# Kernel tuning notes

Hardware: AMD Instinct MI355X
Metric: run time of the kernel (lower is better)

The kernel has to match this reference:

```python
import jax, jax.numpy as jnp
import numpy as np

DIM = 768        # channel dim C
HEADS = 12       # num_heads
MAXLEN = 128     # max_seq_len == window length N
NW = 64          # num_windows
B = 4            # batch


def setup_inputs() -> dict:
    key = jax.random.key(0)
    k0, k1, k2, k3 = jax.random.split(key, 4)
    B_ = NW * B
    x = jax.random.normal(k0, (B_, MAXLEN, DIM), jnp.float32)
    mask = jnp.zeros((NW, MAXLEN, MAXLEN), jnp.float32)  # 0/-inf additive window mask
    qkv_w = jax.random.normal(k1, (3 * DIM, DIM), jnp.float32) * 0.02
    bias_table = jax.random.normal(k2, (2 * MAXLEN - 1, HEADS), jnp.float32) * 0.02
    proj_w = jax.random.normal(k3, (DIM, DIM), jnp.float32) * 0.02
    proj_b = jnp.zeros((DIM,), jnp.float32)
    return {"x": x, "mask": mask, "qkv_w": qkv_w, "bias_table": bias_table,
            "proj_w": proj_w, "proj_b": proj_b}


def reference(x, mask, qkv_w, bias_table, proj_w, proj_b):
    B_, N, C = x.shape
    H = HEADS
    hd = C // H
    scale = hd ** -0.5
    # qkv projection (no bias): (B_, N, 3, H, hd)
    qkv = (x @ qkv_w.T).reshape(B_, N, 3, H, hd)
    q = qkv[:, :, 0].transpose(0, 2, 1, 3) * scale  # (B_, H, N, hd)
    k = qkv[:, :, 1].transpose(0, 2, 1, 3)
    v = qkv[:, :, 2].transpose(0, 2, 1, 3)
    attn = jnp.einsum('bhnd,bhmd->bhnm', q, k)       # (B_, H, N, N)
    # relative position bias gather
    coords = jnp.arange(N)
    rel_idx = coords[:, None] - coords[None, :] + (MAXLEN - 1)  # (N, N)
    bias = bias_table[rel_idx]                        # (N, N, H)
    attn = attn + bias.transpose(2, 0, 1)[None]       # (B_, H, N, N)
    # window mask add (mask ndim == 3 branch)
    nW = mask.shape[0]
    attn = attn.reshape(B_ // nW, nW, H, N, N) + mask[None, :, None]
    attn = jax.nn.softmax(attn.reshape(B_, H, N, N), axis=-1)
    out = jnp.einsum('bhnm,bhmd->bhnd', attn, v)      # (B_, H, N, hd)
    out = out.transpose(0, 2, 1, 3).reshape(B_, N, C)
    return out @ proj_w.T + proj_b
```

## Files before the change

kernel.cpp:

```cpp
#include <hip/hip_runtime.h>
#include <hip/hip_bf16.h>
#include <stdint.h>

typedef unsigned short u16;
typedef __bf16 bf16x8 __attribute__((ext_vector_type(8)));
typedef float f32x4 __attribute__((ext_vector_type(4)));

__device__ __forceinline__ u16 f2bf(float f) {
  union { float f; uint32_t u; } v; v.f = f;
  uint32_t u = v.u;
  return (u16)((u + 0x7FFFu + ((u >> 16) & 1u)) >> 16);
}

__device__ __forceinline__ f32x4 mfma16(bf16x8 a, bf16x8 b, f32x4 c) {
  return __builtin_amdgcn_mfma_f32_16x16x32_bf16(a, b, c, 0, 0, 0);
}

#define GLOBAL_TO_LDS16(g, l)                                                  \
  __builtin_amdgcn_global_load_lds(                                            \
      (const __attribute__((address_space(1))) void*)(g),                      \
      (__attribute__((address_space(3))) void*)(l), 16, 0, 0)

__device__ __forceinline__ int xcd_swz(int lin, int nwg) {
  return (lin & 7) * (nwg >> 3) + (lin >> 3);
}

__global__ void cvt_bf16_all(const float* __restrict__ x, u16* __restrict__ xb,
                             const float* __restrict__ qw, u16* __restrict__ qwb,
                             const float* __restrict__ pw, u16* __restrict__ pwb) {
  int blk = blockIdx.x;
  const float* src; u16* dst; int i;
  if (blk < 24576)        { src = x;  dst = xb;  i = blk * 256 + threadIdx.x; }
  else if (blk < 26304)   { src = qw; dst = qwb; i = (blk - 24576) * 256 + threadIdx.x; }
  else                    { src = pw; dst = pwb; i = (blk - 26304) * 256 + threadIdx.x; }
  float4 f = ((const float4*)src)[i];
  ushort4 o;
  o.x = f2bf(f.x); o.y = f2bf(f.y); o.z = f2bf(f.z); o.w = f2bf(f.w);
  ((ushort4*)dst)[i] = o;
}

template <bool SWAP>
__global__ __launch_bounds__(256) void qkv_gemm(
    const u16* __restrict__ A, const u16* __restrict__ Bt, int nbase,
    u16* __restrict__ q, u16* __restrict__ k, u16* __restrict__ vT) {
  const int K = 768;
  __shared__ u16 As[128 * 64];
  __shared__ u16 Bs[128 * 64];
  int tid = threadIdx.x;
  int wave = tid >> 6, lane = tid & 63;
  int quad = lane >> 4, lrow = lane & 15;
  int lin = blockIdx.x + gridDim.x * blockIdx.y;
  int swz = xcd_swz(lin, gridDim.x * gridDim.y);
  int bx = swz % gridDim.x, by = swz / gridDim.x;
  int m0 = by * 128, n0 = nbase + bx * 128;
  int wr = (wave >> 1) * 64, wc = (wave & 1) * 64;

  const u16* asrc[4]; const u16* bsrc[4]; int ldst[4];
#pragma unroll
  for (int s = 0; s < 4; s++) {
    int p = (wave * 4 + s) * 64 + lane;
    int row = p >> 3, cp = p & 7;
    int c = cp ^ (row & 7);
    asrc[s] = A + (size_t)(m0 + row) * K + c * 8;
    bsrc[s] = Bt + (size_t)(n0 + row) * K + c * 8;
    ldst[s] = p * 8;
  }
  f32x4 acc[4][4] = {};
  for (int k0 = 0; k0 < K; k0 += 64) {
#pragma unroll
    for (int s = 0; s < 4; s++) {
      GLOBAL_TO_LDS16(asrc[s] + k0, As + ldst[s]);
      GLOBAL_TO_LDS16(bsrc[s] + k0, Bs + ldst[s]);
    }
    __syncthreads();
#pragma unroll
    for (int kk = 0; kk < 2; kk++) {
      bf16x8 am[4], bn[4];
#pragma unroll
      for (int i = 0; i < 4; i++) {
        int r = wr + i * 16 + lrow;
        am[i] = *(const bf16x8*)(As + r * 64 + ((((kk << 2) | quad) ^ (r & 7)) << 3));
      }
#pragma unroll
      for (int j = 0; j < 4; j++) {
        int r = wc + j * 16 + lrow;
        bn[j] = *(const bf16x8*)(Bs + r * 64 + ((((kk << 2) | quad) ^ (r & 7)) << 3));
      }
#pragma unroll
      for (int i = 0; i < 4; i++)
#pragma unroll
        for (int j = 0; j < 4; j++)
          acc[i][j] = SWAP ? mfma16(bn[i], am[j], acc[i][j])
                           : mfma16(am[i], bn[j], acc[i][j]);
    }
    __syncthreads();
  }
  int b = m0 >> 7;
  if (SWAP) {
    int t = n0 / 768;
    float s = (t == 0) ? 0.125f : 1.0f;
    u16* dst = (t == 0) ? q : k;
#pragma unroll
    for (int i = 0; i < 4; i++) {
      int nb = (n0 - t * 768) + wc + i * 16 + quad * 4;
      int h = nb >> 6, d0 = nb & 63;
#pragma unroll
      for (int j = 0; j < 4; j++) {
        int seq = wr + j * 16 + lrow;
        ushort4 o;
        o.x = f2bf(acc[i][j][0] * s); o.y = f2bf(acc[i][j][1] * s);
        o.z = f2bf(acc[i][j][2] * s); o.w = f2bf(acc[i][j][3] * s);
        *(ushort4*)(dst + ((size_t)(b * 12 + h)) * 8192 + seq * 64 + d0) = o;
      }
    }
  } else {
#pragma unroll
    for (int j = 0; j < 4; j++) {
      int nb = (n0 - 1536) + wc + j * 16 + lrow;
      int h = nb >> 6, d = nb & 63;
#pragma unroll
      for (int i = 0; i < 4; i++) {
        int seq0 = wr + i * 16 + quad * 4;
        ushort4 o;
        o.x = f2bf(acc[i][j][0]); o.y = f2bf(acc[i][j][1]);
        o.z = f2bf(acc[i][j][2]); o.w = f2bf(acc[i][j][3]);
        *(ushort4*)(vT + ((size_t)(b * 12 + h)) * 8192 + d * 128 + seq0) = o;
      }
    }
  }
}

__global__ __launch_bounds__(512) void attn_kernel(
    const u16* __restrict__ q, const u16* __restrict__ k, const u16* __restrict__ vT,
    const float* __restrict__ mask, const float* __restrict__ bias_table,
    u16* __restrict__ attn_out) {
  __shared__ u16 smem[2 * 128 * 64];
  __shared__ u16 vTs[64 * 128];
  __shared__ float bias_s[255];
  u16* qs = smem;
  u16* ks = smem + 128 * 64;
  u16* ps = smem;
  int tid = threadIdx.x;
  int wave = tid >> 6, lane = tid & 63;
  int quad = lane >> 4, lrow = lane & 15;
  int bh = xcd_swz(blockIdx.x, gridDim.x);
  int b = bh / 12, h = bh - b * 12;
  int w = b & 63;
  if (tid < 255) bias_s[tid] = bias_table[tid * 12 + h];
  const u16* qg = q + (size_t)bh * 8192;
  const u16* kg = k + (size_t)bh * 8192;
  const u16* vg = vT + (size_t)bh * 8192;
#pragma unroll
  for (int s = 0; s < 2; s++) {
    int p = s * 512 + tid;
    int row = p >> 3, c = (p & 7) ^ (row & 7);
    GLOBAL_TO_LDS16(qg + row * 64 + c * 8, qs + p * 8);
    GLOBAL_TO_LDS16(kg + row * 64 + c * 8, ks + p * 8);
    int dd = p >> 4, cv = (p & 15) ^ (dd & 7);
    GLOBAL_TO_LDS16(vg + dd * 128 + cv * 8, vTs + p * 8);
  }
  __syncthreads();

  int row = wave * 16 + lrow;
  f32x4 sacc[8] = {};
#pragma unroll
  for (int kk = 0; kk < 2; kk++) {
    bf16x8 qf = *(const bf16x8*)(qs + row * 64 + ((((kk << 2) | quad) ^ (row & 7)) << 3));
#pragma unroll
    for (int i = 0; i < 8; i++) {
      int rk = i * 16 + lrow;
      bf16x8 kf = *(const bf16x8*)(ks + rk * 64 + ((((kk << 2) | quad) ^ (rk & 7)) << 3));
      sacc[i] = mfma16(kf, qf, sacc[i]);
    }
  }
  const float* mrow = mask + (size_t)w * 16384 + row * 128;
#pragma unroll
  for (int i = 0; i < 8; i++) {
    int c0 = i * 16 + quad * 4;
    float4 m4 = *(const float4*)(mrow + c0);
    sacc[i][0] += bias_s[row - (c0 + 0) + 127] + m4.x;
    sacc[i][1] += bias_s[row - (c0 + 1) + 127] + m4.y;
    sacc[i][2] += bias_s[row - (c0 + 2) + 127] + m4.z;
    sacc[i][3] += bias_s[row - (c0 + 3) + 127] + m4.w;
  }
  float mx = sacc[0][0];
#pragma unroll
  for (int i = 0; i < 8; i++)
#pragma unroll
    for (int r = 0; r < 4; r++) mx = fmaxf(mx, sacc[i][r]);
  mx = fmaxf(mx, __shfl_xor(mx, 16, 64));
  mx = fmaxf(mx, __shfl_xor(mx, 32, 64));
  float sum = 0.f;
#pragma unroll
  for (int i = 0; i < 8; i++)
#pragma unroll
    for (int r = 0; r < 4; r++) {
      float e = __expf(sacc[i][r] - mx);
      sacc[i][r] = e;
      sum += e;
    }
  sum += __shfl_xor(sum, 16, 64);
  sum += __shfl_xor(sum, 32, 64);
  float inv = 1.f / sum;
  __syncthreads();
#pragma unroll
  for (int i = 0; i < 8; i++) {
    int chunk = i * 2 + (quad >> 1);
    int pos = chunk ^ (row & 7);
    ushort4 o;
    o.x = f2bf(sacc[i][0] * inv); o.y = f2bf(sacc[i][1] * inv);
    o.z = f2bf(sacc[i][2] * inv); o.w = f2bf(sacc[i][3] * inv);
    *(ushort4*)(ps + row * 128 + pos * 8 + (quad & 1) * 4) = o;
  }
  __syncthreads();

  f32x4 oacc[4] = {};
#pragma unroll
  for (int kk = 0; kk < 4; kk++) {
    bf16x8 pf = *(const bf16x8*)(ps + row * 128 + ((((kk << 2) | quad) ^ (row & 7)) << 3));
#pragma unroll
    for (int jd = 0; jd < 4; jd++) {
      int rd = jd * 16 + lrow;
      bf16x8 vf = *(const bf16x8*)(vTs + rd * 128 + ((((kk << 2) | quad) ^ (rd & 7)) << 3));
      oacc[jd] = mfma16(vf, pf, oacc[jd]);
    }
  }
#pragma unroll
  for (int jd = 0; jd < 4; jd++) {
    int d0 = jd * 16 + quad * 4;
    int seq = wave * 16 + lrow;
    ushort4 o;
    o.x = f2bf(oacc[jd][0]); o.y = f2bf(oacc[jd][1]);
    o.z = f2bf(oacc[jd][2]); o.w = f2bf(oacc[jd][3]);
    *(ushort4*)(attn_out + ((size_t)(b * 128 + seq)) * 768 + h * 64 + d0) = o;
  }
}

__global__ __launch_bounds__(256) void proj_gemm(
    const u16* __restrict__ A, const u16* __restrict__ Bt,
    const float* __restrict__ bias, float* __restrict__ out) {
  const int K = 768;
  __shared__ u16 As[128 * 64];
  __shared__ u16 Bs[128 * 64];
  int tid = threadIdx.x;
  int wave = tid >> 6, lane = tid & 63;
  int quad = lane >> 4, lrow = lane & 15;
  int lin = blockIdx.x + gridDim.x * blockIdx.y;
  int swz = xcd_swz(lin, gridDim.x * gridDim.y);
  int bx = swz % gridDim.x, by = swz / gridDim.x;
  int m0 = by * 128, n0 = bx * 128;
  int wr = (wave >> 1) * 64, wc = (wave & 1) * 64;

  const u16* asrc[4]; const u16* bsrc[4]; int ldst[4];
#pragma unroll
  for (int s = 0; s < 4; s++) {
    int p = (wave * 4 + s) * 64 + lane;
    int row = p >> 3, c = (p & 7) ^ (row & 7);
    asrc[s] = A + (size_t)(m0 + row) * K + c * 8;
    bsrc[s] = Bt + (size_t)(n0 + row) * K + c * 8;
    ldst[s] = p * 8;
  }
  f32x4 acc[4][4] = {};
  for (int k0 = 0; k0 < K; k0 += 64) {
#pragma unroll
    for (int s = 0; s < 4; s++) {
      GLOBAL_TO_LDS16(asrc[s] + k0, As + ldst[s]);
      GLOBAL_TO_LDS16(bsrc[s] + k0, Bs + ldst[s]);
    }
    __syncthreads();
#pragma unroll
    for (int kk = 0; kk < 2; kk++) {
      bf16x8 am[4], bn[4];
#pragma unroll
      for (int i = 0; i < 4; i++) {
        int r = wr + i * 16 + lrow;
        am[i] = *(const bf16x8*)(As + r * 64 + ((((kk << 2) | quad) ^ (r & 7)) << 3));
      }
#pragma unroll
      for (int j = 0; j < 4; j++) {
        int r = wc + j * 16 + lrow;
        bn[j] = *(const bf16x8*)(Bs + r * 64 + ((((kk << 2) | quad) ^ (r & 7)) << 3));
      }
#pragma unroll
      for (int i = 0; i < 4; i++)
#pragma unroll
        for (int j = 0; j < 4; j++)
          acc[i][j] = mfma16(bn[i], am[j], acc[i][j]);
    }
    __syncthreads();
  }
#pragma unroll
  for (int i = 0; i < 4; i++) {
    int nb = n0 + wc + i * 16 + quad * 4;
    float4 b4 = *(const float4*)(bias + nb);
#pragma unroll
    for (int j = 0; j < 4; j++) {
      int m = m0 + wr + j * 16 + lrow;
      float4 o;
      o.x = acc[i][j][0] + b4.x; o.y = acc[i][j][1] + b4.y;
      o.z = acc[i][j][2] + b4.z; o.w = acc[i][j][3] + b4.w;
      *(float4*)(out + (size_t)m * 768 + nb) = o;
    }
  }
}

extern "C" void kernel_launch(void* const* d_in, const int* in_sizes, int n_in,
                              void* d_out, int out_size, void* d_ws, size_t ws_size,
                              hipStream_t stream) {
  const float* x          = (const float*)d_in[0];
  const float* mask       = (const float*)d_in[1];
  const float* qkv_w      = (const float*)d_in[2];
  const float* bias_table = (const float*)d_in[3];
  const float* proj_w     = (const float*)d_in[4];
  const float* proj_b     = (const float*)d_in[5];
  float* out = (float*)d_out;
  char* ws = (char*)d_ws;
  u16* q_b    = (u16*)(ws);
  u16* k_b    = (u16*)(ws + 50331648);
  u16* vT_b   = (u16*)(ws + 100663296);
  u16* x_b    = (u16*)(ws + 150994944);
  u16* qw_b   = (u16*)(ws + 201326592);
  u16* pw_b   = (u16*)(ws + 204865536);
  u16* attn_b = x_b;

  cvt_bf16_all<<<26880, 256, 0, stream>>>(x, x_b, qkv_w, qw_b, proj_w, pw_b);
  qkv_gemm<true><<<dim3(12, 256), 256, 0, stream>>>(x_b, qw_b, 0, q_b, k_b, vT_b);
  qkv_gemm<false><<<dim3(6, 256), 256, 0, stream>>>(x_b, qw_b, 1536, q_b, k_b, vT_b);
  attn_kernel<<<3072, 512, 0, stream>>>(q_b, k_b, vT_b, mask, bias_table, attn_b);
  proj_gemm<<<dim3(6, 256), 256, 0, stream>>>(attn_b, pw_b, proj_b, out);
}
```

Baseline: 444.2 us.

## Enlarge GEMM M-tile to 256 rows and prefetch mask before attention loads

The QKV and projection GEMMs now use 256x128 tiles instead of 128x128, with each wave computing a 128x64 sub-tile (8x4 MFMA accumulators). This raises arithmetic intensity per LDS load and halves the grid, aiming to cut global and LDS traffic per FLOP. The cost is more accumulator registers (lower occupancy) and more LDS per block. Separately, the attention kernel issues its mask loads at kernel start so their latency overlaps the Q/K/V staging into LDS.

```diff
diff --git a/kernel.cpp b/kernel.cpp
--- a/kernel.cpp
+++ b/kernel.cpp
@@ -44,7 +44,7 @@
     const u16* __restrict__ A, const u16* __restrict__ Bt, int nbase,
     u16* __restrict__ q, u16* __restrict__ k, u16* __restrict__ vT) {
   const int K = 768;
-  __shared__ u16 As[128 * 64];
+  __shared__ u16 As[256 * 64];
   __shared__ u16 Bs[128 * 64];
   int tid = threadIdx.x;
   int wave = tid >> 6, lane = tid & 63;
@@ -52,79 +52,85 @@
   int lin = blockIdx.x + gridDim.x * blockIdx.y;
   int swz = xcd_swz(lin, gridDim.x * gridDim.y);
   int bx = swz % gridDim.x, by = swz / gridDim.x;
-  int m0 = by * 128, n0 = nbase + bx * 128;
-  int wr = (wave >> 1) * 64, wc = (wave & 1) * 64;
-
-  const u16* asrc[4]; const u16* bsrc[4]; int ldst[4];
+  int m0 = by * 256, n0 = nbase + bx * 128;
+  int wm = wave >> 1, wn = wave & 1;
+
+  const u16* asrc[8]; int adst[8];
+#pragma unroll
+  for (int s = 0; s < 8; s++) {
+    int p = s * 256 + tid;
+    int row = p >> 3, c = (p & 7) ^ (row & 7);
+    asrc[s] = A + (size_t)(m0 + row) * K + c * 8;
+    adst[s] = p * 8;
+  }
+  const u16* bsrc[4]; int bdst[4];
 #pragma unroll
   for (int s = 0; s < 4; s++) {
-    int p = (wave * 4 + s) * 64 + lane;
-    int row = p >> 3, cp = p & 7;
-    int c = cp ^ (row & 7);
-    asrc[s] = A + (size_t)(m0 + row) * K + c * 8;
+    int p = s * 256 + tid;
+    int row = p >> 3, c = (p & 7) ^ (row & 7);
     bsrc[s] = Bt + (size_t)(n0 + row) * K + c * 8;
-    ldst[s] = p * 8;
-  }
-  f32x4 acc[4][4] = {};
+    bdst[s] = p * 8;
+  }
+  f32x4 acc[8][4] = {};
   for (int k0 = 0; k0 < K; k0 += 64) {
 #pragma unroll
-    for (int s = 0; s < 4; s++) {
-      GLOBAL_TO_LDS16(asrc[s] + k0, As + ldst[s]);
-      GLOBAL_TO_LDS16(bsrc[s] + k0, Bs + ldst[s]);
-    }
+    for (int s = 0; s < 8; s++) GLOBAL_TO_LDS16(asrc[s] + k0, As + adst[s]);
+#pragma unroll
+    for (int s = 0; s < 4; s++) GLOBAL_TO_LDS16(bsrc[s] + k0, Bs + bdst[s]);
     __syncthreads();
 #pragma unroll
     for (int kk = 0; kk < 2; kk++) {
-      bf16x8 am[4], bn[4];
-#pragma unroll
-      for (int i = 0; i < 4; i++) {
-        int r = wr + i * 16 + lrow;
-        am[i] = *(const bf16x8*)(As + r * 64 + ((((kk << 2) | quad) ^ (r & 7)) << 3));
-      }
-#pragma unroll
-      for (int j = 0; j < 4; j++) {
-        int r = wc + j * 16 + lrow;
-        bn[j] = *(const bf16x8*)(Bs + r * 64 + ((((kk << 2) | quad) ^ (r & 7)) << 3));
-      }
-#pragma unroll
-      for (int i = 0; i < 4; i++)
-#pragma unroll
-        for (int j = 0; j < 4; j++)
-          acc[i][j] = SWAP ? mfma16(bn[i], am[j], acc[i][j])
-                           : mfma16(am[i], bn[j], acc[i][j]);
+      bf16x8 am[8], bn[4];
+#pragma unroll
+      for (int m = 0; m < 8; m++) {
+        int r = wm * 128 + m * 16 + lrow;
+        am[m] = *(const bf16x8*)(As + r * 64 + ((((kk << 2) | quad) ^ (r & 7)) << 3));
+      }
+#pragma unroll
+      for (int n = 0; n < 4; n++) {
+        int r = wn * 64 + n * 16 + lrow;
+        bn[n] = *(const bf16x8*)(Bs + r * 64 + ((((kk << 2) | quad) ^ (r & 7)) << 3));
+      }
+#pragma unroll
+      for (int m = 0; m < 8; m++)
+#pragma unroll
+        for (int n = 0; n < 4; n++)
+          acc[m][n] = SWAP ? mfma16(bn[n], am[m], acc[m][n])
+                           : mfma16(am[m], bn[n], acc[m][n]);
     }
     __syncthreads();
   }
-  int b = m0 >> 7;
   if (SWAP) {
-    int t = n0 / 768;
-    float s = (t == 0) ? 0.125f : 1.0f;
-    u16* dst = (t == 0) ? q : k;
-#pragma unroll
-    for (int i = 0; i < 4; i++) {
-      int nb = (n0 - t * 768) + wc + i * 16 + quad * 4;
-      int h = nb >> 6, d0 = nb & 63;
-#pragma unroll
-      for (int j = 0; j < 4; j++) {
-        int seq = wr + j * 16 + lrow;
+    int t = n0 >= 768;
+    float sc = t ? 1.0f : 0.125f;
+    u16* dst = t ? k : q;
+#pragma unroll
+    for (int n = 0; n < 4; n++) {
+      int f = (n0 - (t ? 768 : 0)) + wn * 64 + n * 16 + quad * 4;
+      int h = f >> 6, d0 = f & 63;
+#pragma unroll
+      for (int m = 0; m < 8; m++) {
+        int seqg = m0 + wm * 128 + m * 16 + lrow;
+        int b = seqg >> 7, s = seqg & 127;
         ushort4 o;
-        o.x = f2bf(acc[i][j][0] * s); o.y = f2bf(acc[i][j][1] * s);
-        o.z = f2bf(acc[i][j][2] * s); o.w = f2bf(acc[i][j][3] * s);
-        *(ushort4*)(dst + ((size_t)(b * 12 + h)) * 8192 + seq * 64 + d0) = o;
+        o.x = f2bf(acc[m][n][0] * sc); o.y = f2bf(acc[m][n][1] * sc);
+        o.z = f2bf(acc[m][n][2] * sc); o.w = f2bf(acc[m][n][3] * sc);
+        *(ushort4*)(dst + ((size_t)(b * 12 + h)) * 8192 + s * 64 + d0) = o;
       }
     }
   } else {
 #pragma unroll
-    for (int j = 0; j < 4; j++) {
-      int nb = (n0 - 1536) + wc + j * 16 + lrow;
+    for (int n = 0; n < 4; n++) {
+      int nb = (n0 - 1536) + wn * 64 + n * 16 + lrow;
       int h = nb >> 6, d = nb & 63;
 #pragma unroll
-      for (int i = 0; i < 4; i++) {
-        int seq0 = wr + i * 16 + quad * 4;
+      for (int m = 0; m < 8; m++) {
+        int seq0 = m0 + wm * 128 + m * 16 + quad * 4;
+        int b = seq0 >> 7, s0 = seq0 & 127;
         ushort4 o;
-        o.x = f2bf(acc[i][j][0]); o.y = f2bf(acc[i][j][1]);
-        o.z = f2bf(acc[i][j][2]); o.w = f2bf(acc[i][j][3]);
-        *(ushort4*)(vT + ((size_t)(b * 12 + h)) * 8192 + d * 128 + seq0) = o;
+        o.x = f2bf(acc[m][n][0]); o.y = f2bf(acc[m][n][1]);
+        o.z = f2bf(acc[m][n][2]); o.w = f2bf(acc[m][n][3]);
+        *(ushort4*)(vT + ((size_t)(b * 12 + h)) * 8192 + d * 128 + s0) = o;
       }
     }
   }
@@ -146,6 +152,13 @@
   int bh = xcd_swz(blockIdx.x, gridDim.x);
   int b = bh / 12, h = bh - b * 12;
   int w = b & 63;
+  int row = wave * 16 + lrow;
+
+  const float* mrow = mask + (size_t)w * 16384 + row * 128;
+  float4 m4[8];
+#pragma unroll
+  for (int i = 0; i < 8; i++) m4[i] = *(const float4*)(mrow + i * 16 + quad * 4);
+
   if (tid < 255) bias_s[tid] = bias_table[tid * 12 + h];
   const u16* qg = q + (size_t)bh * 8192;
   const u16* kg = k + (size_t)bh * 8192;
@@ -153,15 +166,14 @@
 #pragma unroll
   for (int s = 0; s < 2; s++) {
     int p = s * 512 + tid;
-    int row = p >> 3, c = (p & 7) ^ (row & 7);
-    GLOBAL_TO_LDS16(qg + row * 64 + c * 8, qs + p * 8);
-    GLOBAL_TO_LDS16(kg + row * 64 + c * 8, ks + p * 8);
+    int prow = p >> 3, c = (p & 7) ^ (prow & 7);
+    GLOBAL_TO_LDS16(qg + prow * 64 + c * 8, qs + p * 8);
+    GLOBAL_TO_LDS16(kg + prow * 64 + c * 8, ks + p * 8);
     int dd = p >> 4, cv = (p & 15) ^ (dd & 7);
     GLOBAL_TO_LDS16(vg + dd * 128 + cv * 8, vTs + p * 8);
   }
   __syncthreads();
 
-  int row = wave * 16 + lrow;
   f32x4 sacc[8] = {};
 #pragma unroll
   for (int kk = 0; kk < 2; kk++) {
@@ -173,15 +185,13 @@
       sacc[i] = mfma16(kf, qf, sacc[i]);
     }
   }
-  const float* mrow = mask + (size_t)w * 16384 + row * 128;
 #pragma unroll
   for (int i = 0; i < 8; i++) {
     int c0 = i * 16 + quad * 4;
-    float4 m4 = *(const float4*)(mrow + c0);
-    sacc[i][0] += bias_s[row - (c0 + 0) + 127] + m4.x;
-    sacc[i][1] += bias_s[row - (c0 + 1) + 127] + m4.y;
-    sacc[i][2] += bias_s[row - (c0 + 2) + 127] + m4.z;
-    sacc[i][3] += bias_s[row - (c0 + 3) + 127] + m4.w;
+    sacc[i][0] += bias_s[row - (c0 + 0) + 127] + m4[i].x;
+    sacc[i][1] += bias_s[row - (c0 + 1) + 127] + m4[i].y;
+    sacc[i][2] += bias_s[row - (c0 + 2) + 127] + m4[i].z;
+    sacc[i][3] += bias_s[row - (c0 + 3) + 127] + m4[i].w;
   }
   float mx = sacc[0][0];
 #pragma unroll
@@ -240,7 +250,7 @@
     const u16* __restrict__ A, const u16* __restrict__ Bt,
     const float* __restrict__ bias, float* __restrict__ out) {
   const int K = 768;
-  __shared__ u16 As[128 * 64];
+  __shared__ u16 As[256 * 64];
   __shared__ u16 Bs[128 * 64];
   int tid = threadIdx.x;
   int wave = tid >> 6, lane = tid & 63;
@@ -248,58 +258,64 @@
   int lin = blockIdx.x + gridDim.x * blockIdx.y;
   int swz = xcd_swz(lin, gridDim.x * gridDim.y);
   int bx = swz % gridDim.x, by = swz / gridDim.x;
-  int m0 = by * 128, n0 = bx * 128;
-  int wr = (wave >> 1) * 64, wc = (wave & 1) * 64;
-
-  const u16* asrc[4]; const u16* bsrc[4]; int ldst[4];
-#pragma unroll
-  for (int s = 0; s < 4; s++) {
-    int p = (wave * 4 + s) * 64 + lane;
+  int m0 = by * 256, n0 = bx * 128;
+  int wm = wave >> 1, wn = wave & 1;
+
+  const u16* asrc[8]; int adst[8];
+#pragma unroll
+  for (int s = 0; s < 8; s++) {
+    int p = s * 256 + tid;
     int row = p >> 3, c = (p & 7) ^ (row & 7);
     asrc[s] = A + (size_t)(m0 + row) * K + c * 8;
+    adst[s] = p * 8;
+  }
+  const u16* bsrc[4]; int bdst[4];
+#pragma unroll
+  for (int s = 0; s < 4; s++) {
+    int p = s * 256 + tid;
+    int row = p >> 3, c = (p & 7) ^ (row & 7);
     bsrc[s] = Bt + (size_t)(n0 + row) * K + c * 8;
-    ldst[s] = p * 8;
-  }
-  f32x4 acc[4][4] = {};
+    bdst[s] = p * 8;
+  }
+  f32x4 acc[8][4] = {};
   for (int k0 = 0; k0 < K; k0 += 64) {
 #pragma unroll
-    for (int s = 0; s < 4; s++) {
-      GLOBAL_TO_LDS16(asrc[s] + k0, As + ldst[s]);
-      GLOBAL_TO_LDS16(bsrc[s] + k0, Bs + ldst[s]);
-    }
+    for (int s = 0; s < 8; s++) GLOBAL_TO_LDS16(asrc[s] + k0, As + adst[s]);
+#pragma unroll
+    for (int s = 0; s < 4; s++) GLOBAL_TO_LDS16(bsrc[s] + k0, Bs + bdst[s]);
     __syncthreads();
 #pragma unroll
     for (int kk = 0; kk < 2; kk++) {
-      bf16x8 am[4], bn[4];
-#pragma unroll
-      for (int i = 0; i < 4; i++) {
-        int r = wr + i * 16 + lrow;
-        am[i] = *(const bf16x8*)(As + r * 64 + ((((kk << 2) | quad) ^ (r & 7)) << 3));
-      }
-#pragma unroll
-      for (int j = 0; j < 4; j++) {
-        int r = wc + j * 16 + lrow;
-        bn[j] = *(const bf16x8*)(Bs + r * 64 + ((((kk << 2) | quad) ^ (r & 7)) << 3));
-      }
-#pragma unroll
-      for (int i = 0; i < 4; i++)
-#pragma unroll
-        for (int j = 0; j < 4; j++)
-          acc[i][j] = mfma16(bn[i], am[j], acc[i][j]);
+      bf16x8 am[8], bn[4];
+#pragma unroll
+      for (int m = 0; m < 8; m++) {
+        int r = wm * 128 + m * 16 + lrow;
+        am[m] = *(const bf16x8*)(As + r * 64 + ((((kk << 2) | quad) ^ (r & 7)) << 3));
+      }
+#pragma unroll
+      for (int n = 0; n < 4; n++) {
+        int r = wn * 64 + n * 16 + lrow;
+        bn[n] = *(const bf16x8*)(Bs + r * 64 + ((((kk << 2) | quad) ^ (r & 7)) << 3));
+      }
+#pragma unroll
+      for (int m = 0; m < 8; m++)
+#pragma unroll
+        for (int n = 0; n < 4; n++)
+          acc[m][n] = mfma16(bn[n], am[m], acc[m][n]);
     }
     __syncthreads();
   }
 #pragma unroll
-  for (int i = 0; i < 4; i++) {
-    int nb = n0 + wc + i * 16 + quad * 4;
+  for (int n = 0; n < 4; n++) {
+    int nb = n0 + wn * 64 + n * 16 + quad * 4;
     float4 b4 = *(const float4*)(bias + nb);
 #pragma unroll
-    for (int j = 0; j < 4; j++) {
-      int m = m0 + wr + j * 16 + lrow;
+    for (int m = 0; m < 8; m++) {
+      int mr = m0 + wm * 128 + m * 16 + lrow;
       float4 o;
-      o.x = acc[i][j][0] + b4.x; o.y = acc[i][j][1] + b4.y;
-      o.z = acc[i][j][2] + b4.z; o.w = acc[i][j][3] + b4.w;
-      *(float4*)(out + (size_t)m * 768 + nb) = o;
+      o.x = acc[m][n][0] + b4.x; o.y = acc[m][n][1] + b4.y;
+      o.z = acc[m][n][2] + b4.z; o.w = acc[m][n][3] + b4.w;
+      *(float4*)(out + (size_t)mr * 768 + nb) = o;
     }
   }
 }
@@ -324,8 +340,8 @@
   u16* attn_b = x_b;
 
   cvt_bf16_all<<<26880, 256, 0, stream>>>(x, x_b, qkv_w, qw_b, proj_w, pw_b);
-  qkv_gemm<true><<<dim3(12, 256), 256, 0, stream>>>(x_b, qw_b, 0, q_b, k_b, vT_b);
-  qkv_gemm<false><<<dim3(6, 256), 256, 0, stream>>>(x_b, qw_b, 1536, q_b, k_b, vT_b);
+  qkv_gemm<true><<<dim3(12, 128), 256, 0, stream>>>(x_b, qw_b, 0, q_b, k_b, vT_b);
+  qkv_gemm<false><<<dim3(6, 128), 256, 0, stream>>>(x_b, qw_b, 1536, q_b, k_b, vT_b);
   attn_kernel<<<3072, 512, 0, stream>>>(q_b, k_b, vT_b, mask, bias_table, attn_b);
-  proj_gemm<<<dim3(6, 256), 256, 0, stream>>>(attn_b, pw_b, proj_b, out);
-}
+  proj_gemm<<<dim3(6, 128), 256, 0, stream>>>(attn_b, pw_b, proj_b, out);
+}
```

New measurement: 558.0 us. 25.6% more time.
